# Performance work log

Measured on AMD Instinct MI355X. Metric: run time of the kernel, lower is better.

The kernel has to match this reference:

```python
import jax, jax.numpy as jnp
import numpy as np

ALPHA = 0.2  # LeakyReLU negative slope
NEG_INF = -9.0e15


def setup_inputs() -> dict:
    key = jax.random.key(0)
    k1, k2, k3, k4 = jax.random.split(key, 4)
    B, T, N, Fin, Fout = 2, 8, 2048, 64, 64
    h = jax.random.normal(k1, (B, T, N, Fin), dtype=jnp.float32)
    # xavier_uniform-like init for W [Fin,Fout] and a [2*Fout,1]
    limW = 1.414 * np.sqrt(6.0 / (Fin + Fout))
    W = jax.random.uniform(k2, (Fin, Fout), minval=-limW, maxval=limW, dtype=jnp.float32)
    lima = 1.414 * np.sqrt(6.0 / (2 * Fout + 1))
    a = jax.random.uniform(k3, (2 * Fout, 1), minval=-lima, maxval=lima, dtype=jnp.float32)
    adj = jax.random.randint(k4, (N, N), 0, 2).astype(jnp.int32)
    return {"h": h, "W": W, "a": a, "adj": adj}


def reference(h, W, a, adj):
    Fout = W.shape[1]
    Wh = jnp.matmul(h, W)                      # [B,T,N,Fout]
    Wh1 = jnp.matmul(Wh, a[:Fout])             # [B,T,N,1]
    Wh2 = jnp.matmul(Wh, a[Fout:])             # [B,T,N,1]
    e = Wh1 + jnp.swapaxes(Wh2, -1, -2)        # [B,T,N,N]
    e = jnp.where(e > 0, e, ALPHA * e)         # LeakyReLU
    e = jnp.where(adj > 0, e, jnp.float32(NEG_INF))  # adjacency mask
    # NOTE: source does F.softmax(dim=1) -> softmax over the T axis, replicated faithfully
    attention = jax.nn.softmax(e, axis=1)
    # dropout omitted (eval-mode reference)
    out = jnp.matmul(attention, Wh)            # [B,T,N,Fout]
    return jax.nn.elu(out)                     # concat=True
```

## Files before the change

kernel.cpp:

```cpp
#include <hip/hip_runtime.h>
#include <math.h>

#define B_ 2
#define T_ 8
#define N_ 2048
#define F_ 64
#define TI 64
#define JC 64
#define JCP 72
#define LOG2E 1.44269504088896f
#define PART_STRIDE ((size_t)B_ * T_ * N_ * F_)

typedef __attribute__((ext_vector_type(8))) short short8;
typedef __attribute__((ext_vector_type(4))) float f32x4;

__device__ __forceinline__ unsigned short f2bf(float x) {
  unsigned u = __float_as_uint(x);
  u += 0x7FFFu + ((u >> 16) & 1u);
  return (unsigned short)(u >> 16);
}

__device__ __forceinline__ unsigned cvt_pk_bf16(float lo, float hi) {
  unsigned r;
  asm("v_cvt_pk_bf16_f32 %0, %1, %2" : "=v"(r) : "v"(lo), "v"(hi));
  return r;
}

__device__ __forceinline__ float bf2f(unsigned short u) {
  return __uint_as_float(((unsigned)u) << 16);
}

__global__ __launch_bounds__(256) void prep_kernel(
    const float* __restrict__ h, const float* __restrict__ W,
    const float* __restrict__ a, unsigned short* __restrict__ WhT,
    float* __restrict__ U1, float* __restrict__ V1,
    float* __restrict__ U2, float* __restrict__ V2) {
  __shared__ float Ws[64][64];
  __shared__ float hs[64][64];
  __shared__ float Whs[64][65];
  const int tid = threadIdx.x;
  const int row0 = blockIdx.x * 64;
  const int bt = row0 >> 11;
  const int j0 = row0 & 2047;
  for (int i = tid; i < 1024; i += 256)
    ((f32x4*)Ws)[i] = ((const f32x4*)W)[i];
  for (int i = tid; i < 1024; i += 256)
    ((f32x4*)hs)[i] = ((const f32x4*)(h + (size_t)row0 * 64))[i];
  __syncthreads();
  const int f = tid & 63;
  const int rq = tid >> 6;
  float acc[16];
#pragma unroll
  for (int m = 0; m < 16; ++m) acc[m] = 0.f;
#pragma unroll 4
  for (int k = 0; k < 64; ++k) {
    const float wvv = Ws[k][f];
#pragma unroll
    for (int m = 0; m < 16; ++m) acc[m] = fmaf(hs[rq * 16 + m][k], wvv, acc[m]);
  }
#pragma unroll
  for (int m = 0; m < 16; ++m) Whs[rq * 16 + m][f] = acc[m];
  __syncthreads();
  {
    const int r = tid >> 2, q = tid & 3;
    float s1 = 0.f, s2 = 0.f;
#pragma unroll
    for (int k = 0; k < 16; ++k) {
      const float v = Whs[r][q * 16 + k];
      s1 = fmaf(v, a[q * 16 + k], s1);
      s2 = fmaf(v, a[64 + q * 16 + k], s2);
    }
    s1 += __shfl_xor(s1, 1); s1 += __shfl_xor(s1, 2);
    s2 += __shfl_xor(s2, 1); s2 += __shfl_xor(s2, 2);
    if (q == 0) {
      const float z1 = s1 * LOG2E, z2 = s2 * LOG2E;
      const size_t idx = (size_t)bt * N_ + j0 + r;
      U1[idx] = __builtin_amdgcn_exp2f(z1);
      V1[idx] = __builtin_amdgcn_exp2f(0.2f * z1);
      U2[idx] = __builtin_amdgcn_exp2f(z2);
      V2[idx] = __builtin_amdgcn_exp2f(0.2f * z2);
    }
  }
  {
    const int ff = tid & 63, cp = tid >> 6;
#pragma unroll
    for (int cc = 0; cc < 2; ++cc) {
      const int c = cp * 2 + cc;
      short8 v;
#pragma unroll
      for (int k = 0; k < 8; ++k) v[k] = (short)f2bf(Whs[c * 8 + k][ff]);
      *(short8*)(WhT + ((size_t)bt * 64 + ff) * N_ + j0 + c * 8) = v;
    }
  }
}

__global__ __launch_bounds__(1024, 4) void gat_mfma(
    const unsigned short* __restrict__ WhT,
    const float* __restrict__ U1, const float* __restrict__ V1,
    const float* __restrict__ U2, const float* __restrict__ V2,
    const int* __restrict__ adj,
    unsigned short* __restrict__ parts, const int njq) {
  __shared__ unsigned short atts[2][T_][TI][JCP];
  __shared__ float uv2s[2][2][T_][JC];
  const int tid = threadIdx.x;
  const int jq = blockIdx.x % njq;
  const int rest = blockIdx.x / njq;
  const int i0 = (rest & 31) * TI;
  const int b = rest >> 5;
  const int jspan = N_ / njq;
  const int jbase = jq * jspan;
  const int nchunk = jspan / JC;

  const int wv = tid >> 6;
  const int t = wv & 7;
  const int fh = wv >> 3;
  const int lane = tid & 63;
  const int col = lane & 15;
  const int kg = lane >> 4;

  const int sii = tid >> 4;
  const int sjj = (tid & 15) * 4;
  const int stab = tid >> 9, stt = (tid >> 6) & 7, sjn = tid & 63;

  const unsigned short* wtb = WhT + (size_t)(b * T_ + t) * F_ * N_;
  const float* uvsrc = (stab ? V2 : U2) + (size_t)(b * T_ + stt) * N_;
  const int* adjrow = adj + (size_t)(i0 + sii) * N_ + jbase;

  float u1r[T_], v1r[T_];
#pragma unroll
  for (int tt = 0; tt < T_; ++tt) {
    u1r[tt] = U1[(size_t)(b * T_ + tt) * N_ + i0 + sii];
    v1r[tt] = V1[(size_t)(b * T_ + tt) * N_ + i0 + sii];
  }

  f32x4 acc[4][2];
#pragma unroll
  for (int it = 0; it < 4; ++it)
#pragma unroll
    for (int nt = 0; nt < 2; ++nt) acc[it][nt] = {0.f, 0.f, 0.f, 0.f};

  uv2s[0][stab][stt][sjn] = uvsrc[jbase + sjn];
  int4 ad = *(const int4*)(adjrow + sjj);
  __syncthreads();

  for (int c = 0; c < nchunk; ++c) {
    const int j0 = jbase + c * JC;
    const int buf = c & 1;
    short8 breg[2][2];
#pragma unroll
    for (int nt = 0; nt < 2; ++nt)
#pragma unroll
      for (int ks = 0; ks < 2; ++ks)
        breg[nt][ks] = *(const short8*)(wtb + (size_t)(fh * 32 + nt * 16 + col) * N_ +
                                        j0 + ks * 32 + kg * 8);
    if (c + 1 < nchunk)
      uv2s[buf ^ 1][stab][stt][sjn] = uvsrc[j0 + JC + sjn];
    int4 adn = ad;
    if (c + 1 < nchunk) adn = *(const int4*)(adjrow + (c + 1) * JC + sjj);

    unsigned pk[T_][2];
    {
      float e[T_][4];
      f32x4 s = {0.f, 0.f, 0.f, 0.f};
#pragma unroll
      for (int tt = 0; tt < T_; ++tt) {
        const f32x4 qu = *(const f32x4*)(&uv2s[buf][0][tt][sjj]);
        const f32x4 qv = *(const f32x4*)(&uv2s[buf][1][tt][sjj]);
#pragma unroll
        for (int cc = 0; cc < 4; ++cc) {
          const float x = fmaxf(u1r[tt] * qu[cc], v1r[tt] * qv[cc]);
          e[tt][cc] = x;
          s[cc] += x;
        }
      }
      const int adc[4] = {ad.x, ad.y, ad.z, ad.w};
      float rr[4], dd[4];
#pragma unroll
      for (int cc = 0; cc < 4; ++cc) {
        rr[cc] = adc[cc] > 0 ? __builtin_amdgcn_rcpf(s[cc]) : 0.f;
        dd[cc] = adc[cc] > 0 ? 0.f : 0.125f;
      }
#pragma unroll
      for (int tt = 0; tt < T_; ++tt) {
        pk[tt][0] = cvt_pk_bf16(fmaf(e[tt][0], rr[0], dd[0]),
                                fmaf(e[tt][1], rr[1], dd[1]));
        pk[tt][1] = cvt_pk_bf16(fmaf(e[tt][2], rr[2], dd[2]),
                                fmaf(e[tt][3], rr[3], dd[3]));
      }
    }
    ad = adn;
#pragma unroll
    for (int tt = 0; tt < T_; ++tt)
      *(uint2*)&atts[buf][tt][sii][sjj] = make_uint2(pk[tt][0], pk[tt][1]);
    __syncthreads();
#pragma unroll
    for (int it = 0; it < 4; ++it) {
      const unsigned short* ab = &atts[buf][t][it * 16 + col][kg * 8];
      const short8 a0 = *(const short8*)ab;
      const short8 a1 = *(const short8*)(ab + 32);
#pragma unroll
      for (int nt = 0; nt < 2; ++nt) {
        acc[it][nt] = __builtin_amdgcn_mfma_f32_16x16x32_bf16(a0, breg[nt][0], acc[it][nt], 0, 0, 0);
        acc[it][nt] = __builtin_amdgcn_mfma_f32_16x16x32_bf16(a1, breg[nt][1], acc[it][nt], 0, 0, 0);
      }
    }
  }

  unsigned short* ob = parts + (size_t)jq * PART_STRIDE +
                       ((size_t)(b * T_ + t) * N_ + i0) * F_;
#pragma unroll
  for (int it = 0; it < 4; ++it) {
#pragma unroll
    for (int nt = 0; nt < 2; ++nt) {
#pragma unroll
      for (int r = 0; r < 4; ++r) {
        const int row = it * 16 + kg * 4 + r;
        const float x = acc[it][nt][r];
        ob[(size_t)row * F_ + fh * 32 + nt * 16 + col] = (unsigned short)cvt_pk_bf16(x, x);
      }
    }
  }
}

__global__ __launch_bounds__(256) void combine_elu(
    float* __restrict__ out, const unsigned short* __restrict__ parts,
    const int njq) {
  const size_t i = ((size_t)blockIdx.x * 256 + threadIdx.x) * 16;
  float s[16];
#pragma unroll
  for (int k = 0; k < 16; ++k) s[k] = 0.f;
  for (int p = 0; p < njq; ++p) {
    const unsigned short* pp = parts + (size_t)p * PART_STRIDE + i;
    const short8 v0 = *(const short8*)(pp);
    const short8 v1 = *(const short8*)(pp + 8);
#pragma unroll
    for (int k = 0; k < 8; ++k) {
      s[k]     += bf2f((unsigned short)v0[k]);
      s[8 + k] += bf2f((unsigned short)v1[k]);
    }
  }
#pragma unroll
  for (int q = 0; q < 4; ++q) {
    f32x4 r;
#pragma unroll
    for (int k = 0; k < 4; ++k) {
      const float x = s[q * 4 + k];
      r[k] = x > 0.f ? x : expm1f(x);
    }
    *(f32x4*)(out + i + q * 4) = r;
  }
}

extern "C" void kernel_launch(void* const* d_in, const int* in_sizes, int n_in,
                              void* d_out, int out_size, void* d_ws, size_t ws_size,
                              hipStream_t stream) {
  const float* h   = (const float*)d_in[0];
  const float* W   = (const float*)d_in[1];
  const float* a   = (const float*)d_in[2];
  const int*   adj = (const int*)d_in[3];
  float* out = (float*)d_out;

  const size_t whtBytes = (size_t)B_ * T_ * F_ * N_ * 2;
  const size_t vBytes   = (size_t)B_ * T_ * N_ * 4;
  const size_t partB    = PART_STRIDE * 2;

  unsigned short* WhT = (unsigned short*)d_ws;
  float* U1 = (float*)((char*)d_ws + whtBytes);
  float* V1 = U1 + (size_t)B_ * T_ * N_;
  float* U2 = V1 + (size_t)B_ * T_ * N_;
  float* V2 = U2 + (size_t)B_ * T_ * N_;
  unsigned short* parts = (unsigned short*)(V2 + (size_t)B_ * T_ * N_);

  const size_t fixed = whtBytes + 4 * vBytes;
  const int njq = (ws_size >= fixed + 4 * partB) ? 4
                : (ws_size >= fixed + 2 * partB) ? 2 : 1;

  hipLaunchKernelGGL(prep_kernel, dim3(B_ * T_ * N_ / 64), dim3(256), 0, stream,
                     h, W, a, WhT, U1, V1, U2, V2);
  hipLaunchKernelGGL(gat_mfma, dim3(B_ * (N_ / TI) * njq), dim3(1024), 0, stream,
                     WhT, U1, V1, U2, V2, adj, parts, njq);
  hipLaunchKernelGGL(combine_elu, dim3((unsigned)(PART_STRIDE / (256 * 16))), dim3(256),
                     0, stream, out, parts, njq);
}
```

Before: 52.24 us.

## Precompute masked softmax reciprocal matrix and build attention in MFMA register layout

Adds a dsum_kernel that computes, per (b,i,j), the masked reciprocal of the softmax denominator over T and stores it as a bf16 matrix. gat_mfma then stages only this reciprocal tile in LDS and recomputes each attention value directly in MFMA A-fragment registers, so the large per-T attention tile no longer has to go through LDS. It also allows njq=8 when the workspace is big enough. The cost is an extra kernel launch, a 16 MB bf16 intermediate that must be written and read back, and redundant exp-product work across waves. Zero-testing the bf16 reciprocal to decide masking could misfire if a reciprocal underflows.

```diff
diff --git a/kernel.cpp b/kernel.cpp
--- a/kernel.cpp
+++ b/kernel.cpp
@@ -7,7 +7,6 @@
 #define F_ 64
 #define TI 64
 #define JC 64
-#define JCP 72
 #define LOG2E 1.44269504088896f
 #define PART_STRIDE ((size_t)B_ * T_ * N_ * F_)
 
@@ -94,14 +93,48 @@
   }
 }
 
+__global__ __launch_bounds__(1024) void dsum_kernel(
+    const float* __restrict__ U1, const float* __restrict__ V1,
+    const float* __restrict__ U2, const float* __restrict__ V2,
+    const int* __restrict__ adj, unsigned short* __restrict__ Rm) {
+  const int tid = threadIdx.x;
+  const int b = blockIdx.x >> 10;
+  const int i = ((blockIdx.x & 1023) << 1) | (tid >> 9);
+  const int j = (tid & 511) * 4;
+
+  float u1r[T_], v1r[T_];
+#pragma unroll
+  for (int t = 0; t < T_; ++t) {
+    u1r[t] = U1[(size_t)(b * T_ + t) * N_ + i];
+    v1r[t] = V1[(size_t)(b * T_ + t) * N_ + i];
+  }
+  f32x4 s = {0.f, 0.f, 0.f, 0.f};
+#pragma unroll
+  for (int t = 0; t < T_; ++t) {
+    const f32x4 uu = *(const f32x4*)(U2 + (size_t)(b * T_ + t) * N_ + j);
+    const f32x4 vv = *(const f32x4*)(V2 + (size_t)(b * T_ + t) * N_ + j);
+#pragma unroll
+    for (int cc = 0; cc < 4; ++cc)
+      s[cc] += fmaxf(u1r[t] * uu[cc], v1r[t] * vv[cc]);
+  }
+  const int4 ad = *(const int4*)(adj + (size_t)i * N_ + j);
+  const float R0 = ad.x > 0 ? __builtin_amdgcn_rcpf(s[0]) : 0.f;
+  const float R1 = ad.y > 0 ? __builtin_amdgcn_rcpf(s[1]) : 0.f;
+  const float R2 = ad.z > 0 ? __builtin_amdgcn_rcpf(s[2]) : 0.f;
+  const float R3 = ad.w > 0 ? __builtin_amdgcn_rcpf(s[3]) : 0.f;
+  uint2 o;
+  o.x = cvt_pk_bf16(R0, R1);
+  o.y = cvt_pk_bf16(R2, R3);
+  *(uint2*)(Rm + ((size_t)b * N_ + i) * N_ + j) = o;
+}
+
 __global__ __launch_bounds__(1024, 4) void gat_mfma(
     const unsigned short* __restrict__ WhT,
     const float* __restrict__ U1, const float* __restrict__ V1,
     const float* __restrict__ U2, const float* __restrict__ V2,
-    const int* __restrict__ adj,
+    const unsigned short* __restrict__ Rm,
     unsigned short* __restrict__ parts, const int njq) {
-  __shared__ unsigned short atts[2][T_][TI][JCP];
-  __shared__ float uv2s[2][2][T_][JC];
+  __shared__ unsigned short Rl[2][TI][72];
   const int tid = threadIdx.x;
   const int jq = blockIdx.x % njq;
   const int rest = blockIdx.x / njq;
@@ -118,19 +151,19 @@
   const int col = lane & 15;
   const int kg = lane >> 4;
 
-  const int sii = tid >> 4;
-  const int sjj = (tid & 15) * 4;
-  const int stab = tid >> 9, stt = (tid >> 6) & 7, sjn = tid & 63;
+  const int ri = tid >> 4;
+  const int rj = (tid & 15) * 4;
+  const unsigned short* rsrc = Rm + ((size_t)b * N_ + i0 + ri) * N_;
 
   const unsigned short* wtb = WhT + (size_t)(b * T_ + t) * F_ * N_;
-  const float* uvsrc = (stab ? V2 : U2) + (size_t)(b * T_ + stt) * N_;
-  const int* adjrow = adj + (size_t)(i0 + sii) * N_ + jbase;
-
-  float u1r[T_], v1r[T_];
-#pragma unroll
-  for (int tt = 0; tt < T_; ++tt) {
-    u1r[tt] = U1[(size_t)(b * T_ + tt) * N_ + i0 + sii];
-    v1r[tt] = V1[(size_t)(b * T_ + tt) * N_ + i0 + sii];
+  const float* u2row = U2 + (size_t)(b * T_ + t) * N_;
+  const float* v2row = V2 + (size_t)(b * T_ + t) * N_;
+
+  float u1r[4], v1r[4];
+#pragma unroll
+  for (int it = 0; it < 4; ++it) {
+    u1r[it] = U1[(size_t)(b * T_ + t) * N_ + i0 + it * 16 + col];
+    v1r[it] = V1[(size_t)(b * T_ + t) * N_ + i0 + it * 16 + col];
   }
 
   f32x4 acc[4][2];
@@ -139,8 +172,7 @@
 #pragma unroll
     for (int nt = 0; nt < 2; ++nt) acc[it][nt] = {0.f, 0.f, 0.f, 0.f};
 
-  uv2s[0][stab][stt][sjn] = uvsrc[jbase + sjn];
-  int4 ad = *(const int4*)(adjrow + sjj);
+  *(uint2*)&Rl[0][ri][rj] = *(const uint2*)(rsrc + jbase + rj);
   __syncthreads();
 
   for (int c = 0; c < nchunk; ++c) {
@@ -154,56 +186,41 @@
         breg[nt][ks] = *(const short8*)(wtb + (size_t)(fh * 32 + nt * 16 + col) * N_ +
                                         j0 + ks * 32 + kg * 8);
     if (c + 1 < nchunk)
-      uv2s[buf ^ 1][stab][stt][sjn] = uvsrc[j0 + JC + sjn];
-    int4 adn = ad;
-    if (c + 1 < nchunk) adn = *(const int4*)(adjrow + (c + 1) * JC + sjj);
-
-    unsigned pk[T_][2];
-    {
-      float e[T_][4];
-      f32x4 s = {0.f, 0.f, 0.f, 0.f};
-#pragma unroll
-      for (int tt = 0; tt < T_; ++tt) {
-        const f32x4 qu = *(const f32x4*)(&uv2s[buf][0][tt][sjj]);
-        const f32x4 qv = *(const f32x4*)(&uv2s[buf][1][tt][sjj]);
-#pragma unroll
-        for (int cc = 0; cc < 4; ++cc) {
-          const float x = fmaxf(u1r[tt] * qu[cc], v1r[tt] * qv[cc]);
-          e[tt][cc] = x;
-          s[cc] += x;
+      *(uint2*)&Rl[buf ^ 1][ri][rj] = *(const uint2*)(rsrc + j0 + JC + rj);
+    f32x4 u2v[2][2], v2v[2][2];
+#pragma unroll
+    for (int ks = 0; ks < 2; ++ks)
+#pragma unroll
+      for (int q = 0; q < 2; ++q) {
+        u2v[ks][q] = *(const f32x4*)(u2row + j0 + ks * 32 + kg * 8 + q * 4);
+        v2v[ks][q] = *(const f32x4*)(v2row + j0 + ks * 32 + kg * 8 + q * 4);
+      }
+#pragma unroll
+    for (int it = 0; it < 4; ++it) {
+      short8 af[2];
+#pragma unroll
+      for (int ks = 0; ks < 2; ++ks) {
+        const short8 Rf = *(const short8*)&Rl[buf][it * 16 + col][ks * 32 + kg * 8];
+        float att[8];
+#pragma unroll
+        for (int k = 0; k < 8; ++k) {
+          const float e = fmaxf(u1r[it] * u2v[ks][k >> 2][k & 3],
+                                v1r[it] * v2v[ks][k >> 2][k & 3]);
+          const float Rv = bf2f((unsigned short)Rf[k]);
+          att[k] = Rv != 0.f ? e * Rv : 0.125f;
         }
+        unsigned au[4];
+#pragma unroll
+        for (int p = 0; p < 4; ++p) au[p] = cvt_pk_bf16(att[2 * p], att[2 * p + 1]);
+        af[ks] = *(short8*)au;
       }
-      const int adc[4] = {ad.x, ad.y, ad.z, ad.w};
-      float rr[4], dd[4];
-#pragma unroll
-      for (int cc = 0; cc < 4; ++cc) {
-        rr[cc] = adc[cc] > 0 ? __builtin_amdgcn_rcpf(s[cc]) : 0.f;
-        dd[cc] = adc[cc] > 0 ? 0.f : 0.125f;
+#pragma unroll
+      for (int nt = 0; nt < 2; ++nt) {
+        acc[it][nt] = __builtin_amdgcn_mfma_f32_16x16x32_bf16(af[0], breg[nt][0], acc[it][nt], 0, 0, 0);
+        acc[it][nt] = __builtin_amdgcn_mfma_f32_16x16x32_bf16(af[1], breg[nt][1], acc[it][nt], 0, 0, 0);
       }
-#pragma unroll
-      for (int tt = 0; tt < T_; ++tt) {
-        pk[tt][0] = cvt_pk_bf16(fmaf(e[tt][0], rr[0], dd[0]),
-                                fmaf(e[tt][1], rr[1], dd[1]));
-        pk[tt][1] = cvt_pk_bf16(fmaf(e[tt][2], rr[2], dd[2]),
-                                fmaf(e[tt][3], rr[3], dd[3]));
-      }
-    }
-    ad = adn;
-#pragma unroll
-    for (int tt = 0; tt < T_; ++tt)
-      *(uint2*)&atts[buf][tt][sii][sjj] = make_uint2(pk[tt][0], pk[tt][1]);
+    }
     __syncthreads();
-#pragma unroll
-    for (int it = 0; it < 4; ++it) {
-      const unsigned short* ab = &atts[buf][t][it * 16 + col][kg * 8];
-      const short8 a0 = *(const short8*)ab;
-      const short8 a1 = *(const short8*)(ab + 32);
-#pragma unroll
-      for (int nt = 0; nt < 2; ++nt) {
-        acc[it][nt] = __builtin_amdgcn_mfma_f32_16x16x32_bf16(a0, breg[nt][0], acc[it][nt], 0, 0, 0);
-        acc[it][nt] = __builtin_amdgcn_mfma_f32_16x16x32_bf16(a1, breg[nt][1], acc[it][nt], 0, 0, 0);
-      }
-    }
   }
 
   unsigned short* ob = parts + (size_t)jq * PART_STRIDE +
@@ -262,6 +279,7 @@
 
   const size_t whtBytes = (size_t)B_ * T_ * F_ * N_ * 2;
   const size_t vBytes   = (size_t)B_ * T_ * N_ * 4;
+  const size_t rmBytes  = (size_t)B_ * N_ * N_ * 2;
   const size_t partB    = PART_STRIDE * 2;
 
   unsigned short* WhT = (unsigned short*)d_ws;
@@ -269,16 +287,20 @@
   float* V1 = U1 + (size_t)B_ * T_ * N_;
   float* U2 = V1 + (size_t)B_ * T_ * N_;
   float* V2 = U2 + (size_t)B_ * T_ * N_;
-  unsigned short* parts = (unsigned short*)(V2 + (size_t)B_ * T_ * N_);
-
-  const size_t fixed = whtBytes + 4 * vBytes;
-  const int njq = (ws_size >= fixed + 4 * partB) ? 4
+  unsigned short* Rm = (unsigned short*)(V2 + (size_t)B_ * T_ * N_);
+  unsigned short* parts = (unsigned short*)((char*)Rm + rmBytes);
+
+  const size_t fixed = whtBytes + 4 * vBytes + rmBytes;
+  const int njq = (ws_size >= fixed + 8 * partB) ? 8
+                : (ws_size >= fixed + 4 * partB) ? 4
                 : (ws_size >= fixed + 2 * partB) ? 2 : 1;
 
   hipLaunchKernelGGL(prep_kernel, dim3(B_ * T_ * N_ / 64), dim3(256), 0, stream,
                      h, W, a, WhT, U1, V1, U2, V2);
+  hipLaunchKernelGGL(dsum_kernel, dim3(B_ * 1024), dim3(1024), 0, stream,
+                     U1, V1, U2, V2, adj, Rm);
   hipLaunchKernelGGL(gat_mfma, dim3(B_ * (N_ / TI) * njq), dim3(1024), 0, stream,
-                     WhT, U1, V1, U2, V2, adj, parts, njq);
+                     WhT, U1, V1, U2, V2, Rm, parts, njq);
   hipLaunchKernelGGL(combine_elu, dim3((unsigned)(PART_STRIDE / (256 * 16))), dim3(256),
                      0, stream, out, parts, njq);
 }
```

Result: slower. 91.34 us (+74.9%).
